# Kernel optimization log

Measured on AMD Instinct MI355X. Metric: run time of the kernel, lower is better.

## Reference

```python
import jax, jax.numpy as jnp
import numpy as np

POOL_D, POOL_H, POOL_W = 4, 7, 7
SPATIAL_SCALE = 0.25
SAMPLING_RATIO = 2


def setup_inputs() -> dict:
    key = jax.random.key(0)
    k1, k2, k3, k4 = jax.random.split(key, 4)
    N, C, D, H, W = 2, 128, 32, 64, 64
    features = jax.random.normal(k1, (N, C, D, H, W), dtype=jnp.float32)
    R = 256
    inv = 1.0 / SPATIAL_SCALE  # rois live in image coords; features at stride 4
    batch = jax.random.randint(k2, (R,), 0, N).astype(jnp.float32)
    dims = jnp.array([D, H, W], dtype=jnp.float32)
    starts = jax.random.uniform(k3, (R, 3)) * dims * inv * 0.6
    sizes = (0.1 + 0.3 * jax.random.uniform(k4, (R, 3))) * dims * inv
    z1, y1, x1 = starts[:, 0], starts[:, 1], starts[:, 2]
    z2, y2, x2 = z1 + sizes[:, 0], y1 + sizes[:, 1], x1 + sizes[:, 2]
    # roi layout: (batch_idx, x1, y1, z1, x2, y2, z2)
    rois = jnp.stack([batch, x1, y1, z1, x2, y2, z2], axis=1).astype(jnp.float32)
    return {"features": features, "rois": rois}


def _axis(coords, size):
    # classic RoIAlign border handling: outside [-1, size] -> 0 contribution
    valid = (coords >= -1.0) & (coords <= float(size))
    c = jnp.clip(coords, 0.0, float(size) - 1.0)
    lo = jnp.floor(c)
    hi = jnp.minimum(lo + 1.0, float(size) - 1.0)
    w = c - lo  # weight of the hi corner
    return lo.astype(jnp.int32), hi.astype(jnp.int32), w, valid


def roi_align_3d(features, rois):
    N, C, D, H, W = features.shape
    R = rois.shape[0]
    sr = SAMPLING_RATIO
    b = rois[:, 0].astype(jnp.int32)
    x1 = rois[:, 1] * SPATIAL_SCALE
    y1 = rois[:, 2] * SPATIAL_SCALE
    z1 = rois[:, 3] * SPATIAL_SCALE
    x2 = rois[:, 4] * SPATIAL_SCALE
    y2 = rois[:, 5] * SPATIAL_SCALE
    z2 = rois[:, 6] * SPATIAL_SCALE
    rd = jnp.maximum(z2 - z1, 1.0)
    rh = jnp.maximum(y2 - y1, 1.0)
    rw = jnp.maximum(x2 - x1, 1.0)

    def sample_coords(start, extent, P):
        # sampling_ratio sample centers per output bin -> [R, P*sr]
        t = (jnp.arange(P * sr, dtype=jnp.float32) + 0.5) / sr
        return start[:, None] + t[None, :] * (extent / P)[:, None]

    zs = sample_coords(z1, rd, POOL_D)  # [R, SD]
    ys = sample_coords(y1, rh, POOL_H)  # [R, SH]
    xs = sample_coords(x1, rw, POOL_W)  # [R, SW]
    zlo, zhi, wz, vz = _axis(zs, D)
    ylo, yhi, wy, vy = _axis(ys, H)
    xlo, xhi, wx, vx = _axis(xs, W)

    B = b[:, None, None, None]
    Z = lambda a: a[:, :, None, None]
    Y = lambda a: a[:, None, :, None]
    X = lambda a: a[:, None, None, :]

    def g(zi, yi, xi):
        # gather -> [R, SD, SH, SW, C]
        return features[B, :, Z(zi), Y(yi), X(xi)]

    wz1, wy1, wx1 = Z(wz)[..., None], Y(wy)[..., None], X(wx)[..., None]
    wz0, wy0, wx0 = 1.0 - wz1, 1.0 - wy1, 1.0 - wx1
    val = (g(zlo, ylo, xlo) * (wz0 * wy0 * wx0)
           + g(zlo, ylo, xhi) * (wz0 * wy0 * wx1)
           + g(zlo, yhi, xlo) * (wz0 * wy1 * wx0)
           + g(zlo, yhi, xhi) * (wz0 * wy1 * wx1)
           + g(zhi, ylo, xlo) * (wz1 * wy0 * wx0)
           + g(zhi, ylo, xhi) * (wz1 * wy0 * wx1)
           + g(zhi, yhi, xlo) * (wz1 * wy1 * wx0)
           + g(zhi, yhi, xhi) * (wz1 * wy1 * wx1))
    valid = (Z(vz) & Y(vy) & X(vx))[..., None]
    val = jnp.where(valid, val, 0.0)
    # average the sr^3 samples per bin
    val = val.reshape(R, POOL_D, sr, POOL_H, sr, POOL_W, sr, C)
    out = val.mean(axis=(2, 4, 6))  # [R, PD, PH, PW, C]
    return jnp.transpose(out, (0, 4, 1, 2, 3))  # [R, C, PD, PH, PW]


def reference(features, rois):
    return roi_align_3d(features, rois)
```

## Files before the change

kernel.cpp:

```cpp
#include <hip/hip_runtime.h>

constexpr int C_  = 128;
constexpr int D_  = 32;
constexpr int H_  = 64;
constexpr int W_  = 64;
constexpr int PD = 4;
constexpr int PH = 7;
constexpr int PW = 7;
constexpr int SR = 2;
constexpr float SCALE = 0.25f;
constexpr int S_ = D_ * H_ * W_;
constexpr int BINS_PER_ROI = PD * PH * PW;
constexpr int SLAB = PH * PW;

__device__ __forceinline__ void axis2(float start, float extent, int P, int p,
                                      int size, int lo[2], int hi[2],
                                      float w[2], bool v[2]) {
    float bin = extent / (float)P;
#pragma unroll
    for (int u = 0; u < 2; ++u) {
        float t = ((float)(p * SR + u) + 0.5f) / (float)SR;
        float coord = start + t * bin;
        v[u] = (coord >= -1.0f) && (coord <= (float)size);
        float cc = fminf(fmaxf(coord, 0.0f), (float)size - 1.0f);
        float fl = floorf(cc);
        lo[u] = (int)fl;
        hi[u] = min(lo[u] + 1, size - 1);
        w[u] = cc - fl;
    }
}

__device__ __forceinline__ unsigned int f2bf(float f) {
    unsigned int u = __float_as_uint(f);
    u += 0x7fffu + ((u >> 16) & 1u);
    return u >> 16;
}

__device__ __forceinline__ float4 bf4(uint2 v) {
    float4 f;
    f.x = __uint_as_float(v.x << 16);
    f.y = __uint_as_float(v.x & 0xffff0000u);
    f.z = __uint_as_float(v.y << 16);
    f.w = __uint_as_float(v.y & 0xffff0000u);
    return f;
}

__global__ __launch_bounds__(512) void transpose_bf16(
    const float* __restrict__ in, unsigned int* __restrict__ outp) {
    __shared__ unsigned int tileu[128][67];
    const int n  = blockIdx.y;
    const int s0 = blockIdx.x * 128;
    const int t  = threadIdx.x;

    const float* src = in + (size_t)n * C_ * S_;
    unsigned int* dst = outp + (size_t)n * (C_ / 2) * S_;

    {
        const int cp0 = t >> 5;
        const int s4  = (t & 31) * 4;
#pragma unroll
        for (int p = 0; p < 4; ++p) {
            const int cp = cp0 + 16 * p;
            const int c = cp * 2;
            const float4 a = *(const float4*)&src[(size_t)c * S_ + (s0 + s4)];
            const float4 b =
                *(const float4*)&src[(size_t)(c + 1) * S_ + (s0 + s4)];
            tileu[s4 + 0][cp] = f2bf(a.x) | (f2bf(b.x) << 16);
            tileu[s4 + 1][cp] = f2bf(a.y) | (f2bf(b.y) << 16);
            tileu[s4 + 2][cp] = f2bf(a.z) | (f2bf(b.z) << 16);
            tileu[s4 + 3][cp] = f2bf(a.w) | (f2bf(b.w) << 16);
        }
    }
    __syncthreads();
    {
        const int row0 = t >> 5;
        const int cp2  = (t & 31) * 2;
#pragma unroll
        for (int p = 0; p < 8; ++p) {
            const int s = row0 + 16 * p;
            uint2 v;
            v.x = tileu[s][cp2 + 0];
            v.y = tileu[s][cp2 + 1];
            *(uint2*)&dst[(size_t)(s0 + s) * (C_ / 2) + cp2] = v;
        }
    }
}

__global__ __launch_bounds__(512) void roi_align_slab(
    const unsigned short* __restrict__ ft,
    const float* __restrict__ rois,
    float* __restrict__ out,
    int R) {
    __shared__ __align__(16) float tile[SLAB][132];

    int r, pd;
    if ((R & 7) == 0) {
        const int xcd = blockIdx.x & 7;
        const int q = blockIdx.x >> 3;
        pd = q & 3;
        r = ((q >> 2) << 3) + xcd;
    } else {
        r = blockIdx.x >> 2;
        pd = blockIdx.x & 3;
    }

    const int t = threadIdx.x;
    const int grp = t >> 5;
    const int c4 = (t & 31) * 4;

    const float* roi = rois + (size_t)r * 7;
    const int b = (int)roi[0];
    const float x1 = roi[1] * SCALE, y1 = roi[2] * SCALE, z1 = roi[3] * SCALE;
    const float x2 = roi[4] * SCALE, y2 = roi[5] * SCALE, z2 = roi[6] * SCALE;
    const float rd = fmaxf(z2 - z1, 1.0f);
    const float rh = fmaxf(y2 - y1, 1.0f);
    const float rw = fmaxf(x2 - x1, 1.0f);

    int zlo[2], zhi[2];
    float wz[2];
    bool vz[2];
    axis2(z1, rd, PD, pd, D_, zlo, zhi, wz, vz);

#pragma unroll 1
    for (int k = 0; k < 4; ++k) {
        const int slot = grp + 16 * k;
        if (slot < SLAB) {
            const int ph = slot / PW;
            const int pw = slot - ph * PW;

            int ylo[2], yhi[2], xlo[2], xhi[2];
            float wy[2], wx[2];
            bool vy[2], vx[2];
            axis2(y1, rh, PH, ph, H_, ylo, yhi, wy, vy);
            axis2(x1, rw, PW, pw, W_, xlo, xhi, wx, vx);

            float4 acc = make_float4(0.f, 0.f, 0.f, 0.f);
#pragma unroll
            for (int i = 0; i < 2; ++i) {
                if (!vz[i]) continue;
                const float wz1 = wz[i], wz0 = 1.0f - wz1;
#pragma unroll
                for (int j = 0; j < 2; ++j) {
                    if (!vy[j]) continue;
                    const float wy1 = wy[j], wy0 = 1.0f - wy1;
                    const size_t r00 =
                        (((size_t)b * D_ + zlo[i]) * H_ + ylo[j]) * W_;
                    const size_t r10 =
                        (((size_t)b * D_ + zhi[i]) * H_ + ylo[j]) * W_;
                    const size_t r01 =
                        (((size_t)b * D_ + zlo[i]) * H_ + yhi[j]) * W_;
                    const size_t r11 =
                        (((size_t)b * D_ + zhi[i]) * H_ + yhi[j]) * W_;
#pragma unroll
                    for (int kk = 0; kk < 2; ++kk) {
                        if (!vx[kk]) continue;
                        const float wx1 = wx[kk], wx0 = 1.0f - wx1;
                        const size_t xl = xlo[kk], xh = xhi[kk];
                        const float4 f000 =
                            bf4(*(const uint2*)&ft[(r00 + xl) * C_ + c4]);
                        const float4 f001 =
                            bf4(*(const uint2*)&ft[(r00 + xh) * C_ + c4]);
                        const float4 f010 =
                            bf4(*(const uint2*)&ft[(r01 + xl) * C_ + c4]);
                        const float4 f011 =
                            bf4(*(const uint2*)&ft[(r01 + xh) * C_ + c4]);
                        const float4 f100 =
                            bf4(*(const uint2*)&ft[(r10 + xl) * C_ + c4]);
                        const float4 f101 =
                            bf4(*(const uint2*)&ft[(r10 + xh) * C_ + c4]);
                        const float4 f110 =
                            bf4(*(const uint2*)&ft[(r11 + xl) * C_ + c4]);
                        const float4 f111 =
                            bf4(*(const uint2*)&ft[(r11 + xh) * C_ + c4]);
                        const float w000 = wz0 * wy0 * wx0,
                                    w001 = wz0 * wy0 * wx1;
                        const float w010 = wz0 * wy1 * wx0,
                                    w011 = wz0 * wy1 * wx1;
                        const float w100 = wz1 * wy0 * wx0,
                                    w101 = wz1 * wy0 * wx1;
                        const float w110 = wz1 * wy1 * wx0,
                                    w111 = wz1 * wy1 * wx1;
                        acc.x += w000 * f000.x + w001 * f001.x +
                                 w010 * f010.x + w011 * f011.x +
                                 w100 * f100.x + w101 * f101.x +
                                 w110 * f110.x + w111 * f111.x;
                        acc.y += w000 * f000.y + w001 * f001.y +
                                 w010 * f010.y + w011 * f011.y +
                                 w100 * f100.y + w101 * f101.y +
                                 w110 * f110.y + w111 * f111.y;
                        acc.z += w000 * f000.z + w001 * f001.z +
                                 w010 * f010.z + w011 * f011.z +
                                 w100 * f100.z + w101 * f101.z +
                                 w110 * f110.z + w111 * f111.z;
                        acc.w += w000 * f000.w + w001 * f001.w +
                                 w010 * f010.w + w011 * f011.w +
                                 w100 * f100.w + w101 * f101.w +
                                 w110 * f110.w + w111 * f111.w;
                    }
                }
            }
            const float s = 1.0f / (SR * SR * SR);
            acc.x *= s; acc.y *= s; acc.z *= s; acc.w *= s;
            *(float4*)&tile[slot][c4] = acc;
        }
    }

    __syncthreads();

    const size_t obase = (size_t)r * C_ * BINS_PER_ROI + (size_t)pd * SLAB;
#pragma unroll 1
    for (int idx = t; idx < C_ * SLAB; idx += 512) {
        const int c = idx / SLAB;
        const int o = idx - c * SLAB;
        __builtin_nontemporal_store(tile[o][c],
                                    &out[obase + (size_t)c * BINS_PER_ROI + o]);
    }
}

__global__ void roi_align_direct(const float* __restrict__ feat,
                                 const float* __restrict__ rois,
                                 float* __restrict__ out, int total) {
    const int tid = blockIdx.x * blockDim.x + threadIdx.x;
    if (tid >= total) return;
    int t = tid;
    const int pw = t % PW; t /= PW;
    const int ph = t % PH; t /= PH;
    const int pd = t % PD; t /= PD;
    const int c = t % C_;  t /= C_;
    const int r = t;

    const float* roi = rois + (size_t)r * 7;
    const int b = (int)roi[0];
    const float x1 = roi[1] * SCALE, y1 = roi[2] * SCALE, z1 = roi[3] * SCALE;
    const float x2 = roi[4] * SCALE, y2 = roi[5] * SCALE, z2 = roi[6] * SCALE;
    const float rd = fmaxf(z2 - z1, 1.0f);
    const float rh = fmaxf(y2 - y1, 1.0f);
    const float rw = fmaxf(x2 - x1, 1.0f);

    int zlo[2], zhi[2], ylo[2], yhi[2], xlo[2], xhi[2];
    float wz[2], wy[2], wx[2];
    bool vz[2], vy[2], vx[2];
    axis2(z1, rd, PD, pd, D_, zlo, zhi, wz, vz);
    axis2(y1, rh, PH, ph, H_, ylo, yhi, wy, vy);
    axis2(x1, rw, PW, pw, W_, xlo, xhi, wx, vx);

    const float* fc = feat + ((size_t)b * C_ + c) * S_;
    float acc = 0.0f;
#pragma unroll
    for (int i = 0; i < 2; ++i) {
        if (!vz[i]) continue;
#pragma unroll
        for (int j = 0; j < 2; ++j) {
            if (!vy[j]) continue;
            const size_t r00 = ((size_t)zlo[i] * H_ + ylo[j]) * W_;
            const size_t r10 = ((size_t)zhi[i] * H_ + ylo[j]) * W_;
            const size_t r01 = ((size_t)zlo[i] * H_ + yhi[j]) * W_;
            const size_t r11 = ((size_t)zhi[i] * H_ + yhi[j]) * W_;
            const float wz1 = wz[i], wz0 = 1.0f - wz1;
            const float wy1 = wy[j], wy0 = 1.0f - wy1;
#pragma unroll
            for (int k = 0; k < 2; ++k) {
                if (!vx[k]) continue;
                const float wx1 = wx[k], wx0 = 1.0f - wx1;
                acc += wz0 * (wy0 * (wx0 * fc[r00 + xlo[k]] + wx1 * fc[r00 + xhi[k]]) +
                              wy1 * (wx0 * fc[r01 + xlo[k]] + wx1 * fc[r01 + xhi[k]])) +
                       wz1 * (wy0 * (wx0 * fc[r10 + xlo[k]] + wx1 * fc[r10 + xhi[k]]) +
                              wy1 * (wx0 * fc[r11 + xlo[k]] + wx1 * fc[r11 + xhi[k]]));
            }
        }
    }
    out[tid] = acc * (1.0f / (SR * SR * SR));
}

extern "C" void kernel_launch(void* const* d_in, const int* in_sizes, int n_in,
                              void* d_out, int out_size, void* d_ws,
                              size_t ws_size, hipStream_t stream) {
    const float* features = (const float*)d_in[0];
    const float* rois = (const float*)d_in[1];
    float* out = (float*)d_out;

    const int R = in_sizes[1] / 7;
    const int N = in_sizes[0] / (C_ * S_);
    const size_t need = (size_t)in_sizes[0] * sizeof(unsigned short);

    if (ws_size >= need) {
        unsigned short* ft = (unsigned short*)d_ws;

        dim3 tg(S_ / 128, N);
        transpose_bf16<<<tg, 512, 0, stream>>>(features, (unsigned int*)ft);

        roi_align_slab<<<R * PD, 512, 0, stream>>>(ft, rois, out, R);
    } else {
        const int total = R * C_ * BINS_PER_ROI;
        roi_align_direct<<<(total + 255) / 256, 256, 0, stream>>>(
            features, rois, out, total);
    }
}
```

Measured before the change: 264.6 us.

## Widen transpose tile, XOR-swizzle shared memory, use nontemporal loads

The fp32-to-bf16 channel-last transpose kernel now handles 256 spatial positions per block instead of 128, halving the grid. The padded shared tile is replaced by an unpadded one indexed with an XOR swizzle to avoid bank conflicts on both the write and read phases. Source loads use nontemporal hints so the one-time-read feature tensor does not pollute cache. The larger per-thread work raises register use and the swizzle adds index arithmetic.

```diff
diff --git a/kernel.cpp b/kernel.cpp
--- a/kernel.cpp
+++ b/kernel.cpp
@@ -13,6 +13,8 @@
 constexpr int BINS_PER_ROI = PD * PH * PW;
 constexpr int SLAB = PH * PW;
 
+typedef float vf4 __attribute__((ext_vector_type(4)));
+
 __device__ __forceinline__ void axis2(float start, float extent, int P, int p,
                                       int size, int lo[2], int hi[2],
                                       float w[2], bool v[2]) {
@@ -47,40 +49,43 @@
 
 __global__ __launch_bounds__(512) void transpose_bf16(
     const float* __restrict__ in, unsigned int* __restrict__ outp) {
-    __shared__ unsigned int tileu[128][67];
+    __shared__ unsigned int tileu[256][64];
     const int n  = blockIdx.y;
-    const int s0 = blockIdx.x * 128;
+    const int s0 = blockIdx.x * 256;
     const int t  = threadIdx.x;
 
     const float* src = in + (size_t)n * C_ * S_;
     unsigned int* dst = outp + (size_t)n * (C_ / 2) * S_;
 
     {
-        const int cp0 = t >> 5;
-        const int s4  = (t & 31) * 4;
-#pragma unroll
-        for (int p = 0; p < 4; ++p) {
-            const int cp = cp0 + 16 * p;
+        const int sl  = t & 63;
+        const int cp0 = t >> 6;
+#pragma unroll
+        for (int p = 0; p < 8; ++p) {
+            const int cp = cp0 + 8 * p;
             const int c = cp * 2;
-            const float4 a = *(const float4*)&src[(size_t)c * S_ + (s0 + s4)];
-            const float4 b =
-                *(const float4*)&src[(size_t)(c + 1) * S_ + (s0 + s4)];
-            tileu[s4 + 0][cp] = f2bf(a.x) | (f2bf(b.x) << 16);
-            tileu[s4 + 1][cp] = f2bf(a.y) | (f2bf(b.y) << 16);
-            tileu[s4 + 2][cp] = f2bf(a.z) | (f2bf(b.z) << 16);
-            tileu[s4 + 3][cp] = f2bf(a.w) | (f2bf(b.w) << 16);
+            const vf4 a = __builtin_nontemporal_load(
+                (const vf4*)&src[(size_t)c * S_ + (s0 + 4 * sl)]);
+            const vf4 b = __builtin_nontemporal_load(
+                (const vf4*)&src[(size_t)(c + 1) * S_ + (s0 + 4 * sl)]);
+            const int col = cp ^ (sl & 31);
+            tileu[4 * sl + 0][col] = f2bf(a.x) | (f2bf(b.x) << 16);
+            tileu[4 * sl + 1][col] = f2bf(a.y) | (f2bf(b.y) << 16);
+            tileu[4 * sl + 2][col] = f2bf(a.z) | (f2bf(b.z) << 16);
+            tileu[4 * sl + 3][col] = f2bf(a.w) | (f2bf(b.w) << 16);
         }
     }
     __syncthreads();
     {
-        const int row0 = t >> 5;
-        const int cp2  = (t & 31) * 2;
-#pragma unroll
-        for (int p = 0; p < 8; ++p) {
-            const int s = row0 + 16 * p;
+        const int cp2   = (t & 31) * 2;
+        const int rbase = t >> 5;
+#pragma unroll
+        for (int it = 0; it < 16; ++it) {
+            const int s = rbase + 16 * it;
+            const int w = (s >> 2) & 31;
             uint2 v;
-            v.x = tileu[s][cp2 + 0];
-            v.y = tileu[s][cp2 + 1];
+            v.x = tileu[s][cp2 ^ w];
+            v.y = tileu[s][(cp2 + 1) ^ w];
             *(uint2*)&dst[(size_t)(s0 + s) * (C_ / 2) + cp2] = v;
         }
     }
@@ -286,7 +291,7 @@
     if (ws_size >= need) {
         unsigned short* ft = (unsigned short*)d_ws;
 
-        dim3 tg(S_ / 128, N);
+        dim3 tg(S_ / 256, N);
         transpose_bf16<<<tg, 512, 0, stream>>>(features, (unsigned int*)ft);
 
         roi_align_slab<<<R * PD, 512, 0, stream>>>(ft, rois, out, R);
```

Measured after the change: 260.1 us. No clear change (-1.7%).
